# Kernel optimization log

Hardware: AMD Instinct MI355X
Metric: run time of the kernel (lower is better)

The kernel has to match this reference:

```python
import jax, jax.numpy as jnp
import numpy as np

N = 100000      # nodes
E = 1600000     # random edges (self loops added in reference, like add_self_loops)
D_IN = 128
D_OUT = 128
NEG_SLOPE = 0.01  # F.leaky_relu default in the torch source


def setup_inputs() -> dict:
    key = jax.random.key(0)
    k_x, k_e, k_w, k_b, k_a, k_ab = jax.random.split(key, 6)
    x = jax.random.normal(k_x, (N, D_IN), dtype=jnp.float32)
    edge_index = jax.random.randint(k_e, (2, E), 0, N, dtype=jnp.int32)
    # small init scales keep exp(score) in a sane range (torch default init is also small)
    W_lin = jax.random.normal(k_w, (D_OUT, D_IN), dtype=jnp.float32) * 0.05
    b_lin = jax.random.normal(k_b, (D_OUT,), dtype=jnp.float32) * 0.05
    W_att = jax.random.normal(k_a, (1, 2 * D_OUT), dtype=jnp.float32) * 0.05
    b_att = jax.random.normal(k_ab, (1,), dtype=jnp.float32) * 0.05
    return {"x": x, "edge_index": edge_index, "W_lin": W_lin, "b_lin": b_lin,
            "W_att": W_att, "b_att": b_att}


def reference(x, edge_index, W_lin, b_lin, W_att, b_att):
    n = x.shape[0]
    d_out = W_lin.shape[0]
    # h = lin(x), computed ONCE (the torch loop redundantly recomputes it per edge)
    h = x @ W_lin.T + b_lin                      # [N, D_OUT]
    # add self loops (pyg_utils.add_self_loops)
    loops = jnp.arange(n, dtype=edge_index.dtype)
    src = jnp.concatenate([edge_index[0], loops])  # node i (attends over its out-neighbors)
    dst = jnp.concatenate([edge_index[1], loops])  # neighbor j
    # attention([h_i ; h_j]) = h_i . a_i + h_j . a_j + b
    a_i = W_att[0, :d_out]
    a_j = W_att[0, d_out:]
    score = h[src] @ a_i + h[dst] @ a_j + b_att[0]           # [E+N]
    score = jnp.where(score >= 0, score, NEG_SLOPE * score)  # leaky_relu(0.01)
    e = jnp.exp(score)                                        # plain exp, as in source (no max-shift)
    denom = jax.ops.segment_sum(e, src, num_segments=n)       # per-source softmax denominator
    alpha = e / denom[src]                                    # [E+N]
    msg = alpha[:, None] * h[dst]                             # [E+N, D_OUT]
    agg = jax.ops.segment_sum(msg, src, num_segments=n)       # attention_matrix @ h
    return jax.nn.elu(agg)
```

## Files before the change

kernel.cpp:

```cpp
#include <hip/hip_runtime.h>
#include <hip/hip_bf16.h>
#include <stdint.h>

typedef unsigned int uint;
typedef unsigned short ushort;

#define D 128
#define NEG_SLOPE 0.01f
#define BN 64
#define CAP 1280
#define NFILL 256
#define KMAX 2048
#define GSTRIDE 16

using frag_t = __attribute__((ext_vector_type(8))) short;
using f32x4  = __attribute__((ext_vector_type(4))) float;

__device__ __forceinline__ ushort f2bf(float f) {
    __hip_bfloat16 b = __float2bfloat16(f);
    ushort u; __builtin_memcpy(&u, &b, 2); return u;
}
__device__ __forceinline__ float bflo(uint p) { return __uint_as_float(p << 16); }
__device__ __forceinline__ float bfhi(uint p) { return __uint_as_float(p & 0xffff0000u); }

#define LDK 136

__global__ __launch_bounds__(512) void gemm_fill(
    const float* __restrict__ x, const float* __restrict__ W,
    const float* __restrict__ bias, const float* __restrict__ Wa,
    const float* __restrict__ ba,
    const int* __restrict__ src, const int* __restrict__ dst,
    ushort* __restrict__ h, float* __restrict__ si, float* __restrict__ sj,
    int* __restrict__ gcnt, uint* __restrict__ barr,
    int n, int e, int K, int cpb)
{
    __shared__ union {
        ushort wsh[128 * LDK];
        int    cur[KMAX];
    } sm;
    const int tid = threadIdx.x;

    if (blockIdx.x < NFILL) {
        int* cur = sm.cur;
        for (int i = tid; i < K; i += 512) cur[i] = 0;
        __syncthreads();
        const int beg = blockIdx.x * cpb;
        const int end = min(e, beg + cpb);
        for (int i = beg + tid; i < end; i += 512)
            atomicAdd(&cur[src[i] >> 6], 1);
        __syncthreads();
        for (int i = tid; i < K; i += 512) {
            int hc = cur[i];
            cur[i] = hc ? atomicAdd(&gcnt[i * GSTRIDE], hc) : 0;
        }
        __syncthreads();
        for (int i = beg + tid; i < end; i += 512) {
            int s = src[i], d = dst[i];
            int b = s >> 6;
            int p = atomicAdd(&cur[b], 1);
            if (p < CAP)
                barr[(size_t)b * CAP + p] = ((uint)(s & (BN - 1)) << 17) | (uint)d;
        }
        return;
    }

    const int row0 = (blockIdx.x - NFILL) * 128;
    const int wv   = tid >> 6;
    const int lane = tid & 63;
    const int mr   = lane & 15;
    const int qk   = (lane >> 4) * 8;

    {
        const int r = tid >> 5;
        const int k = (tid & 31) * 4;
#pragma unroll
        for (int i = 0; i < 8; ++i) {
            int lr = r + 16 * i;
            float4 v = *(const float4*)(W + lr * D + k);
            ushort4 u; u.x = f2bf(v.x); u.y = f2bf(v.y); u.z = f2bf(v.z); u.w = f2bf(v.w);
            *(ushort4*)&sm.wsh[lr * LDK + k] = u;
        }
    }

    const int arow = row0 + 16 * wv + mr;
    const int crd  = arow < n ? arow : (n - 1);
    const float* xr = x + (size_t)crd * D + qk;
    frag_t af[4];
#pragma unroll
    for (int kk = 0; kk < 4; ++kk) {
        float4 u0 = *(const float4*)(xr + kk * 32);
        float4 u1 = *(const float4*)(xr + kk * 32 + 4);
        union { frag_t f; ushort us[8]; } c;
        c.us[0] = f2bf(u0.x); c.us[1] = f2bf(u0.y); c.us[2] = f2bf(u0.z); c.us[3] = f2bf(u0.w);
        c.us[4] = f2bf(u1.x); c.us[5] = f2bf(u1.y); c.us[6] = f2bf(u1.z); c.us[7] = f2bf(u1.w);
        af[kk] = c.f;
    }
    __syncthreads();

    f32x4 acc[8] = {};
#pragma unroll
    for (int kk = 0; kk < 4; ++kk) {
#pragma unroll
        for (int t = 0; t < 8; ++t) {
            frag_t bf = *(const frag_t*)(sm.wsh + (16 * t + mr) * LDK + kk * 32 + qk);
            acc[t] = __builtin_amdgcn_mfma_f32_16x16x32_bf16(af[kk], bf, acc[t], 0, 0, 0);
        }
    }

    const int crow = 16 * wv + (lane >> 4) * 4;
    float pi[4] = {0.f, 0.f, 0.f, 0.f};
    float pj[4] = {0.f, 0.f, 0.f, 0.f};
#pragma unroll
    for (int t = 0; t < 8; ++t) {
        int col = 16 * t + mr;
        float bb = bias[col];
        float av = Wa[col];
        float bv = Wa[D + col];
#pragma unroll
        for (int r = 0; r < 4; ++r) {
            float v = acc[t][r] + bb;
            int grow = row0 + crow + r;
            if (grow < n) h[(size_t)grow * D + col] = f2bf(v);
            pi[r] += v * av;
            pj[r] += v * bv;
        }
    }
#pragma unroll
    for (int o = 1; o < 16; o <<= 1) {
#pragma unroll
        for (int r = 0; r < 4; ++r) {
            pi[r] += __shfl_xor(pi[r], o);
            pj[r] += __shfl_xor(pj[r], o);
        }
    }
    if (mr == 0) {
        float bav = ba[0];
#pragma unroll
        for (int r = 0; r < 4; ++r) {
            int grow = row0 + crow + r;
            if (grow < n) { si[grow] = pi[r] + bav; sj[grow] = pj[r]; }
        }
    }
}

__global__ __launch_bounds__(512) void agg_k(
    const ushort* __restrict__ h, const uint* __restrict__ barr,
    const int* __restrict__ gcnt,
    const float* __restrict__ si, const float* __restrict__ sj,
    float* __restrict__ out, int n)
{
    __shared__ uint2 se[CAP];
    __shared__ int hist[BN];
    __shared__ int base[BN];
    __shared__ int cur[BN];
    __shared__ float si_s[BN];
    __shared__ float sj_s[BN];
    const int b    = blockIdx.x;
    const int tid  = threadIdx.x;
    const int lane = tid & 63;
    const int wv   = tid >> 6;
    const int node0 = b << 6;

    if (tid < BN) {
        hist[tid] = 0;
        int nd = node0 + tid;
        si_s[tid] = nd < n ? si[nd] : 0.f;
        sj_s[tid] = nd < n ? sj[nd] : 0.f;
    }
    __syncthreads();

    const int ecnt = min(gcnt[b * GSTRIDE], CAP);
    const uint* eb = barr + (size_t)b * CAP;

    uint p0 = 0, p1 = 0, p2 = 0;
    float w0 = 0.f, w1 = 0.f, w2 = 0.f;
    const bool v0 = tid < ecnt, v1 = tid + 512 < ecnt, v2 = tid + 1024 < ecnt;
    if (v0) {
        p0 = eb[tid];
        float sc = si_s[p0 >> 17] + sj[p0 & 0x1FFFFu];
        sc = sc >= 0.f ? sc : NEG_SLOPE * sc;
        w0 = __expf(sc);
        atomicAdd(&hist[p0 >> 17], 1);
    }
    if (v1) {
        p1 = eb[tid + 512];
        float sc = si_s[p1 >> 17] + sj[p1 & 0x1FFFFu];
        sc = sc >= 0.f ? sc : NEG_SLOPE * sc;
        w1 = __expf(sc);
        atomicAdd(&hist[p1 >> 17], 1);
    }
    if (v2) {
        p2 = eb[tid + 1024];
        float sc = si_s[p2 >> 17] + sj[p2 & 0x1FFFFu];
        sc = sc >= 0.f ? sc : NEG_SLOPE * sc;
        w2 = __expf(sc);
        atomicAdd(&hist[p2 >> 17], 1);
    }
    __syncthreads();

    if (tid < 64) {
        int v = hist[tid];
        int s = v;
#pragma unroll
        for (int o = 1; o < 64; o <<= 1) {
            int t = __shfl_up(s, o);
            if (lane >= o) s += t;
        }
        base[tid] = s - v;
        cur[tid]  = s - v;
    }
    __syncthreads();

    if (v0) se[atomicAdd(&cur[p0 >> 17], 1)] = make_uint2(p0, __float_as_uint(w0));
    if (v1) se[atomicAdd(&cur[p1 >> 17], 1)] = make_uint2(p1, __float_as_uint(w1));
    if (v2) se[atomicAdd(&cur[p2 >> 17], 1)] = make_uint2(p2, __float_as_uint(w2));
    __syncthreads();

    const uint lo = (uint)lane << 1;
#pragma unroll 1
    for (int t = 0; t < 8; ++t) {
        const int ls = (wv << 3) + t;
        const int node = node0 + ls;
        if (node >= n) break;

        float sc = si_s[ls] + sj_s[ls];
        sc = sc >= 0.f ? sc : NEG_SLOPE * sc;
        float w_ = __expf(sc);
        uint hv = *(const uint*)(h + (((uint)node << 7) + lo));
        float a0 = w_ * bflo(hv), a1 = w_ * bfhi(hv);
        float denom = w_;

        const int c = hist[ls];
        const uint2* seg = se + base[ls];
        int j = 0;
        for (; j + 4 <= c; j += 4) {
            uint2 w0_ = seg[j], w1_ = seg[j + 1], w2_ = seg[j + 2], w3_ = seg[j + 3];
            uint g0 = *(const uint*)(h + (((w0_.x & 0x1FFFFu) << 7) + lo));
            uint g1 = *(const uint*)(h + (((w1_.x & 0x1FFFFu) << 7) + lo));
            uint g2 = *(const uint*)(h + (((w2_.x & 0x1FFFFu) << 7) + lo));
            uint g3 = *(const uint*)(h + (((w3_.x & 0x1FFFFu) << 7) + lo));
            float e0 = __uint_as_float(w0_.y), e1 = __uint_as_float(w1_.y);
            float e2 = __uint_as_float(w2_.y), e3 = __uint_as_float(w3_.y);
            denom += (e0 + e1) + (e2 + e3);
            a0 += e0 * bflo(g0) + e1 * bflo(g1) + e2 * bflo(g2) + e3 * bflo(g3);
            a1 += e0 * bfhi(g0) + e1 * bfhi(g1) + e2 * bfhi(g2) + e3 * bfhi(g3);
        }
        for (; j < c; ++j) {
            uint2 w = seg[j];
            uint g = *(const uint*)(h + (((w.x & 0x1FFFFu) << 7) + lo));
            float we = __uint_as_float(w.y);
            denom += we;
            a0 += we * bflo(g);
            a1 += we * bfhi(g);
        }

        float inv = 1.f / denom;
        a0 *= inv; a1 *= inv;
        a0 = a0 > 0.f ? a0 : expm1f(a0);
        a1 = a1 > 0.f ? a1 : expm1f(a1);
        *(float2*)(out + (((uint)node << 7) + lo)) = make_float2(a0, a1);
    }
}

extern "C" void kernel_launch(void* const* d_in, const int* in_sizes, int n_in,
                              void* d_out, int out_size, void* d_ws, size_t ws_size,
                              hipStream_t stream)
{
    const float* x  = (const float*)d_in[0];
    const int*   ei = (const int*)  d_in[1];
    const float* Wl = (const float*)d_in[2];
    const float* bl = (const float*)d_in[3];
    const float* Wa = (const float*)d_in[4];
    const float* ba = (const float*)d_in[5];
    const int n = in_sizes[0] / D;
    const int e = in_sizes[1] / 2;
    const int* src = ei;
    const int* dst = ei + e;

    const int K   = (n + BN - 1) / BN;
    const int cpb = (e + NFILL - 1) / NFILL;

    char* w = (char*)d_ws;
    size_t off = 0;
    ushort* h    = (ushort*)(w + off); off += (size_t)n * D * 2;
    float*  si   = (float*) (w + off); off += (size_t)n * 4;
    float*  sj   = (float*) (w + off); off += (size_t)n * 4;
    int*    gcnt = (int*)   (w + off); off += (size_t)K * GSTRIDE * 4;
    uint*   barr = (uint*)  (w + off); off += (size_t)K * CAP * 4;

    const int gblocks = (n + 127) / 128;

    hipMemsetAsync(gcnt, 0, (size_t)K * GSTRIDE * 4, stream);
    gemm_fill <<<NFILL + gblocks, 512, 0, stream>>>(x, Wl, bl, Wa, ba, src, dst,
                                                    h, si, sj, gcnt, barr, n, e, K, cpb);
    agg_k     <<<K,               512, 0, stream>>>(h, barr, gcnt, si, sj, (float*)d_out, n);
}
```

Before: 235.1 us.

## Split wavefront into half-waves gathering 8-byte rows over alternating edges

In the aggregation kernel each wavefront now splits into two 32-lane halves. Each lane loads 8 bytes (4 bf16 channels) per neighbor row instead of 4 bytes, and the two halves handle alternating edges; their partial sums are combined with cross-half shuffles before normalization and ELU. This widens each gather load and doubles the number of independent neighbor rows in flight, aiming to hide gather latency. It also uses packed float2 FMAs and makes the bucket-fill stores nontemporal, at the cost of extra shuffles, a half-wave tail path and half-idle lanes on the output store.

Result: slower. 256.9 us (+9.3%).

```diff
diff --git a/kernel.cpp b/kernel.cpp
--- a/kernel.cpp
+++ b/kernel.cpp
@@ -15,6 +15,7 @@
 
 using frag_t = __attribute__((ext_vector_type(8))) short;
 using f32x4  = __attribute__((ext_vector_type(4))) float;
+using v2f    = __attribute__((ext_vector_type(2))) float;
 
 __device__ __forceinline__ ushort f2bf(float f) {
     __hip_bfloat16 b = __float2bfloat16(f);
@@ -59,7 +60,9 @@
             int b = s >> 6;
             int p = atomicAdd(&cur[b], 1);
             if (p < CAP)
-                barr[(size_t)b * CAP + p] = ((uint)(s & (BN - 1)) << 17) | (uint)d;
+                __builtin_nontemporal_store(
+                    ((uint)(s & (BN - 1)) << 17) | (uint)d,
+                    &barr[(size_t)b * CAP + p]);
         }
         return;
     }
@@ -159,6 +162,8 @@
     const int tid  = threadIdx.x;
     const int lane = tid & 63;
     const int wv   = tid >> 6;
+    const int half = lane >> 5;
+    const int hl   = lane & 31;
     const int node0 = b << 6;
 
     if (tid < BN) {
@@ -216,7 +221,7 @@
     if (v2) se[atomicAdd(&cur[p2 >> 17], 1)] = make_uint2(p2, __float_as_uint(w2));
     __syncthreads();
 
-    const uint lo = (uint)lane << 1;
+    const uint co = (uint)hl << 2;
 #pragma unroll 1
     for (int t = 0; t < 8; ++t) {
         const int ls = (wv << 3) + t;
@@ -225,40 +230,69 @@
 
         float sc = si_s[ls] + sj_s[ls];
         sc = sc >= 0.f ? sc : NEG_SLOPE * sc;
-        float w_ = __expf(sc);
-        uint hv = *(const uint*)(h + (((uint)node << 7) + lo));
-        float a0 = w_ * bflo(hv), a1 = w_ * bfhi(hv);
-        float denom = w_;
+        float ws = half ? 0.f : __expf(sc);
+        uint2 hv = *(const uint2*)(h + (((uint)node << 7) + co));
+        v2f a01 = { ws * bflo(hv.x), ws * bfhi(hv.x) };
+        v2f a23 = { ws * bflo(hv.y), ws * bfhi(hv.y) };
+        float denom = ws;
 
         const int c = hist[ls];
         const uint2* seg = se + base[ls];
         int j = 0;
-        for (; j + 4 <= c; j += 4) {
-            uint2 w0_ = seg[j], w1_ = seg[j + 1], w2_ = seg[j + 2], w3_ = seg[j + 3];
-            uint g0 = *(const uint*)(h + (((w0_.x & 0x1FFFFu) << 7) + lo));
-            uint g1 = *(const uint*)(h + (((w1_.x & 0x1FFFFu) << 7) + lo));
-            uint g2 = *(const uint*)(h + (((w2_.x & 0x1FFFFu) << 7) + lo));
-            uint g3 = *(const uint*)(h + (((w3_.x & 0x1FFFFu) << 7) + lo));
-            float e0 = __uint_as_float(w0_.y), e1 = __uint_as_float(w1_.y);
-            float e2 = __uint_as_float(w2_.y), e3 = __uint_as_float(w3_.y);
-            denom += (e0 + e1) + (e2 + e3);
-            a0 += e0 * bflo(g0) + e1 * bflo(g1) + e2 * bflo(g2) + e3 * bflo(g3);
-            a1 += e0 * bfhi(g0) + e1 * bfhi(g1) + e2 * bfhi(g2) + e3 * bfhi(g3);
-        }
-        for (; j < c; ++j) {
-            uint2 w = seg[j];
-            uint g = *(const uint*)(h + (((w.x & 0x1FFFFu) << 7) + lo));
-            float we = __uint_as_float(w.y);
-            denom += we;
-            a0 += we * bflo(g);
-            a1 += we * bfhi(g);
-        }
+        for (; j + 8 <= c; j += 8) {
+            uint2 e0 = seg[j + 0 + half];
+            uint2 e1 = seg[j + 2 + half];
+            uint2 e2 = seg[j + 4 + half];
+            uint2 e3 = seg[j + 6 + half];
+            uint2 g0 = *(const uint2*)(h + (((e0.x & 0x1FFFFu) << 7) + co));
+            uint2 g1 = *(const uint2*)(h + (((e1.x & 0x1FFFFu) << 7) + co));
+            uint2 g2 = *(const uint2*)(h + (((e2.x & 0x1FFFFu) << 7) + co));
+            uint2 g3 = *(const uint2*)(h + (((e3.x & 0x1FFFFu) << 7) + co));
+            float f0 = __uint_as_float(e0.y), f1 = __uint_as_float(e1.y);
+            float f2 = __uint_as_float(e2.y), f3 = __uint_as_float(e3.y);
+            denom += (f0 + f1) + (f2 + f3);
+            a01 += (v2f){f0, f0} * (v2f){bflo(g0.x), bfhi(g0.x)};
+            a23 += (v2f){f0, f0} * (v2f){bflo(g0.y), bfhi(g0.y)};
+            a01 += (v2f){f1, f1} * (v2f){bflo(g1.x), bfhi(g1.x)};
+            a23 += (v2f){f1, f1} * (v2f){bflo(g1.y), bfhi(g1.y)};
+            a01 += (v2f){f2, f2} * (v2f){bflo(g2.x), bfhi(g2.x)};
+            a23 += (v2f){f2, f2} * (v2f){bflo(g2.y), bfhi(g2.y)};
+            a01 += (v2f){f3, f3} * (v2f){bflo(g3.x), bfhi(g3.x)};
+            a23 += (v2f){f3, f3} * (v2f){bflo(g3.y), bfhi(g3.y)};
+        }
+        for (; j + 2 <= c; j += 2) {
+            uint2 e0 = seg[j + half];
+            uint2 g0 = *(const uint2*)(h + (((e0.x & 0x1FFFFu) << 7) + co));
+            float f0 = __uint_as_float(e0.y);
+            denom += f0;
+            a01 += (v2f){f0, f0} * (v2f){bflo(g0.x), bfhi(g0.x)};
+            a23 += (v2f){f0, f0} * (v2f){bflo(g0.y), bfhi(g0.y)};
+        }
+        if (j < c && half == 0) {
+            uint2 e0 = seg[j];
+            uint2 g0 = *(const uint2*)(h + (((e0.x & 0x1FFFFu) << 7) + co));
+            float f0 = __uint_as_float(e0.y);
+            denom += f0;
+            a01 += (v2f){f0, f0} * (v2f){bflo(g0.x), bfhi(g0.x)};
+            a23 += (v2f){f0, f0} * (v2f){bflo(g0.y), bfhi(g0.y)};
+        }
+
+        denom += __shfl_xor(denom, 32);
+        a01.x += __shfl_xor(a01.x, 32);
+        a01.y += __shfl_xor(a01.y, 32);
+        a23.x += __shfl_xor(a23.x, 32);
+        a23.y += __shfl_xor(a23.y, 32);
 
         float inv = 1.f / denom;
-        a0 *= inv; a1 *= inv;
-        a0 = a0 > 0.f ? a0 : expm1f(a0);
-        a1 = a1 > 0.f ? a1 : expm1f(a1);
-        *(float2*)(out + (((uint)node << 7) + lo)) = make_float2(a0, a1);
+        float4 o;
+        o.x = a01.x * inv; o.y = a01.y * inv;
+        o.z = a23.x * inv; o.w = a23.y * inv;
+        o.x = o.x > 0.f ? o.x : expm1f(o.x);
+        o.y = o.y > 0.f ? o.y : expm1f(o.y);
+        o.z = o.z > 0.f ? o.z : expm1f(o.z);
+        o.w = o.w > 0.f ? o.w : expm1f(o.w);
+        if (half == 0)
+            *(float4*)(out + (((uint)node << 7) + co)) = o;
     }
 }
 
```
